# Optimization experiments

Hardware: AMD Instinct MI355X
Metric: run time of the kernel (lower is better)

Reference implementation:

```python
import jax, jax.numpy as jnp
import numpy as np

N_HEADS = 16
N_UNITS = 1024
B, S = 4, 1024


def setup_inputs() -> dict:
    key = jax.random.key(0)
    ks = jax.random.split(key, 12)
    std = 0.02
    query = jax.random.normal(ks[0], (B, S, N_UNITS), dtype=jnp.float32)
    key_t = jax.random.normal(ks[1], (B, S, N_UNITS), dtype=jnp.float32)
    value = jax.random.normal(ks[2], (B, S, N_UNITS), dtype=jnp.float32)
    # causal mask [B, S, S]; forward does mask.unsqueeze(1) -> broadcast over heads
    mask = jnp.broadcast_to(jnp.tril(jnp.ones((S, S), dtype=jnp.int32)), (B, S, S))
    Wq = jax.random.normal(ks[3], (N_UNITS, N_UNITS), dtype=jnp.float32) * std
    bq = jnp.zeros((N_UNITS,), dtype=jnp.float32)
    Wk = jax.random.normal(ks[4], (N_UNITS, N_UNITS), dtype=jnp.float32) * std
    bk = jnp.zeros((N_UNITS,), dtype=jnp.float32)
    Wv = jax.random.normal(ks[5], (N_UNITS, N_UNITS), dtype=jnp.float32) * std
    bv = jnp.zeros((N_UNITS,), dtype=jnp.float32)
    Wo = jax.random.normal(ks[6], (N_UNITS, N_UNITS), dtype=jnp.float32) * std
    bo = jnp.zeros((N_UNITS,), dtype=jnp.float32)
    return {"query": query, "key": key_t, "value": value, "mask": mask,
            "Wq": Wq, "bq": bq, "Wk": Wk, "bk": bk, "Wv": Wv, "bv": bv,
            "Wo": Wo, "bo": bo}


def reference(query, key, value, mask, Wq, bq, Wk, bk, Wv, bv, Wo, bo):
    b, s, u = query.shape
    h = N_HEADS
    dk = u // h
    # projections (torch Linear: x @ W.T + b), split into heads -> [b, h, s, dk]
    q = (query @ Wq.T + bq).reshape(b, s, h, dk).transpose(0, 2, 1, 3)
    k = (key @ Wk.T + bk).reshape(b, s, h, dk).transpose(0, 2, 1, 3)
    v = (value @ Wv.T + bv).reshape(b, s, h, dk).transpose(0, 2, 1, 3)
    # NOTE: original divides by sqrt(d_k) twice -> net scale 1/d_k (faithful)
    scores = jnp.einsum('bhqd,bhkd->bhqk', q, k) / jnp.float32(dk)
    scores = jnp.where(mask[:, None, :, :] == 0, jnp.float32(-1e9), scores)
    attn = jax.nn.softmax(scores, axis=-1)  # dropout = identity (eval mode)
    out = jnp.einsum('bhqk,bhkd->bhqd', attn, v)
    out = out.transpose(0, 2, 1, 3).reshape(b, s, u)
    return out @ Wo.T + bo
```

## Files before the change

kernel.cpp:

```cpp
#include <hip/hip_runtime.h>
#include <stdint.h>

#define NH 16
#define DK 64
#define NB 4
#define SS 1024
#define UU 1024

typedef __attribute__((ext_vector_type(8))) __bf16 bf16x8;
typedef __attribute__((ext_vector_type(4))) float f32x4;

__device__ inline short f2bf(float f) {
  union { float f; uint32_t u; } c; c.f = f;
  uint32_t u = c.u;
  uint32_t r = (u + 0x7fffu + ((u >> 16) & 1u)) >> 16;
  return (short)(uint16_t)r;
}

__global__ void cvt_multi(const float* __restrict__ s0, const float* __restrict__ s1,
                          const float* __restrict__ s2, const float* __restrict__ s3,
                          short* __restrict__ dst, int n4each) {
  const int z = blockIdx.z;
  const float* s = (z == 0) ? s0 : (z == 1) ? s1 : (z == 2) ? s2 : s3;
  int i = blockIdx.x * blockDim.x + threadIdx.x;
  if (i >= n4each) return;
  const float4 v = reinterpret_cast<const float4*>(s)[i];
  short4 o;
  o.x = f2bf(v.x); o.y = f2bf(v.y); o.z = f2bf(v.z); o.w = f2bf(v.w);
  reinterpret_cast<short4*>(dst + (size_t)z * n4each * 4)[i] = o;
}

template <int ROWS>
__device__ inline void stage_rows(short* lds, const short* gsrc, int ld) {
  const int t = threadIdx.x;
  const int w = t >> 6;
  constexpr int ROUNDS = ROWS / 64;
#pragma unroll
  for (int r = 0; r < ROUNDS; ++r) {
    int idx = r * 256 + t;
    const short* src = gsrc + (size_t)(idx >> 2) * ld + (idx & 3) * 8;
    __builtin_amdgcn_global_load_lds(
        (const __attribute__((address_space(1))) void*)src,
        (__attribute__((address_space(3))) void*)(lds + (size_t)(r * 256 + (w << 6)) * 8),
        16, 0, 0);
  }
}

#define BK 32
#define QSCALE 0.015625f

__global__ void gemm_qkv(const float* __restrict__ xq, const float* __restrict__ xk,
                         const float* __restrict__ xv, const short* __restrict__ wq,
                         const short* __restrict__ wk, const short* __restrict__ wv,
                         const float* __restrict__ bq, const float* __restrict__ bk,
                         const float* __restrict__ bv, short* __restrict__ qb,
                         short* __restrict__ kb, short* __restrict__ vT) {
  __shared__ short As[128 * BK];
  __shared__ short Bs[128 * BK];
  const int bid = blockIdx.x;
  const int g = bid & 7, s2 = bid >> 3;
  const int P = g + (s2 >> 3) * 8;
  const int xt = s2 & 7;
  const int which = P >> 5;
  const int m0 = (P & 31) * 128;
  const int n0 = xt * 128;

  const float* A = (which == 0) ? xq : (which == 1) ? xk : xv;
  const short* Bt = ((which == 0) ? wq : (which == 1) ? wk : wv) + (size_t)n0 * UU;
  const float* bias = (which == 0) ? bq : (which == 1) ? bk : bv;

  const int t = threadIdx.x;
  const int w = t >> 6, l = t & 63, lg = l >> 4, lr = l & 15;
  const int wr = w >> 1, wc = w & 1;

  f32x4 acc[4][4];
#pragma unroll
  for (int i = 0; i < 4; ++i)
#pragma unroll
    for (int j = 0; j < 4; ++j) acc[i][j] = (f32x4){0.f, 0.f, 0.f, 0.f};

  float4 ar[2][2];
  auto loadA = [&](int k0) {
#pragma unroll
    for (int r = 0; r < 2; ++r) {
      const int idx = r * 256 + t;
      const float* s = A + (size_t)(m0 + (idx >> 2)) * UU + k0 + (idx & 3) * 8;
      ar[r][0] = reinterpret_cast<const float4*>(s)[0];
      ar[r][1] = reinterpret_cast<const float4*>(s)[1];
    }
  };
  loadA(0);

  for (int k0 = 0; k0 < UU; k0 += BK) {
    asm volatile("s_waitcnt vmcnt(0)" ::: "memory");
    __builtin_amdgcn_sched_barrier(0);
#pragma unroll
    for (int r = 0; r < 2; ++r) {
      const int idx = r * 256 + t;
      bf16x8 os;
      os[0] = (__bf16)ar[r][0].x; os[1] = (__bf16)ar[r][0].y;
      os[2] = (__bf16)ar[r][0].z; os[3] = (__bf16)ar[r][0].w;
      os[4] = (__bf16)ar[r][1].x; os[5] = (__bf16)ar[r][1].y;
      os[6] = (__bf16)ar[r][1].z; os[7] = (__bf16)ar[r][1].w;
      *reinterpret_cast<bf16x8*>(&As[idx * 8]) = os;
    }
    __builtin_amdgcn_sched_barrier(0);
    stage_rows<128>(Bs, Bt + k0, UU);
    __builtin_amdgcn_sched_barrier(0);
    const int kn = k0 + BK;
    if (kn < UU) {
      loadA(kn);
      __builtin_amdgcn_sched_barrier(0);
      asm volatile("s_waitcnt vmcnt(4) lgkmcnt(0)" ::: "memory");
    } else {
      asm volatile("s_waitcnt vmcnt(0) lgkmcnt(0)" ::: "memory");
    }
    __builtin_amdgcn_sched_barrier(0);
    __builtin_amdgcn_s_barrier();
    __builtin_amdgcn_sched_barrier(0);

    bf16x8 af[4], bfr[4];
#pragma unroll
    for (int i = 0; i < 4; ++i)
      af[i] = *(const bf16x8*)&As[(wr * 64 + i * 16 + lr) * BK + lg * 8];
#pragma unroll
    for (int j = 0; j < 4; ++j)
      bfr[j] = *(const bf16x8*)&Bs[(wc * 64 + j * 16 + lr) * BK + lg * 8];
#pragma unroll
    for (int i = 0; i < 4; ++i)
#pragma unroll
      for (int j = 0; j < 4; ++j)
        acc[i][j] = __builtin_amdgcn_mfma_f32_16x16x32_bf16(af[i], bfr[j], acc[i][j], 0, 0, 0);
    __builtin_amdgcn_sched_barrier(0);
    __builtin_amdgcn_s_barrier();
  }

#pragma unroll
  for (int i = 0; i < 4; ++i) {
#pragma unroll
    for (int j = 0; j < 4; ++j) {
      const int col = n0 + wc * 64 + j * 16 + lr;
      const float bv2 = bias[col];
#pragma unroll
      for (int r = 0; r < 4; ++r) {
        const int row = m0 + wr * 64 + i * 16 + lg * 4 + r;
        float v = acc[i][j][r] + bv2;
        if (which == 0) v *= QSCALE;
        const int b = row >> 10, s = row & 1023;
        const int h = col >> 6, d = col & 63;
        if (which < 2) {
          short* outp = (which == 0) ? qb : kb;
          outp[((size_t)(b * NH + h) * SS + s) * DK + d] = f2bf(v);
        } else {
          vT[((size_t)(b * NH + h) * DK + d) * SS + s] = f2bf(v);
        }
      }
    }
  }
}

__global__ void gemm_out(const short* __restrict__ A, const short* __restrict__ Bt,
                         const float* __restrict__ bias, float* __restrict__ out,
                         int M, int N, int K) {
  __shared__ short As[128 * BK];
  __shared__ short Bs[64 * BK];
  const int bid = blockIdx.x;
  const int g = bid & 7, s2 = bid >> 3;
  const int y = g + (s2 >> 4) * 8;
  const int xt = s2 & 15;
  const int m0 = y * 128, n0 = xt * 64;

  const int t = threadIdx.x;
  const int w = t >> 6, l = t & 63, lg = l >> 4, lr = l & 15;
  const int wr = w >> 1, wc = w & 1;

  f32x4 acc[4][2];
#pragma unroll
  for (int i = 0; i < 4; ++i)
#pragma unroll
    for (int j = 0; j < 2; ++j) acc[i][j] = (f32x4){0.f, 0.f, 0.f, 0.f};

  for (int k0 = 0; k0 < K; k0 += BK) {
    stage_rows<128>(As, A + (size_t)m0 * K + k0, K);
    stage_rows<64>(Bs, Bt + (size_t)n0 * K + k0, K);
    __syncthreads();
    bf16x8 af[4], bfr[2];
#pragma unroll
    for (int i = 0; i < 4; ++i)
      af[i] = *(const bf16x8*)&As[(wr * 64 + i * 16 + lr) * BK + lg * 8];
#pragma unroll
    for (int j = 0; j < 2; ++j)
      bfr[j] = *(const bf16x8*)&Bs[(wc * 32 + j * 16 + lr) * BK + lg * 8];
#pragma unroll
    for (int i = 0; i < 4; ++i)
#pragma unroll
      for (int j = 0; j < 2; ++j)
        acc[i][j] = __builtin_amdgcn_mfma_f32_16x16x32_bf16(af[i], bfr[j], acc[i][j], 0, 0, 0);
    __syncthreads();
  }

#pragma unroll
  for (int i = 0; i < 4; ++i) {
#pragma unroll
    for (int j = 0; j < 2; ++j) {
      const int col = n0 + wc * 32 + j * 16 + lr;
      const float bv = bias[col];
#pragma unroll
      for (int r = 0; r < 4; ++r) {
        const int row = m0 + wr * 64 + i * 16 + lg * 4 + r;
        out[(size_t)row * N + col] = acc[i][j][r] + bv;
      }
    }
  }
}

__global__ void attn_fused(const short* __restrict__ Qh, const short* __restrict__ Kh,
                           const short* __restrict__ VT, short* __restrict__ Ctx) {
  __shared__ short Ks[2][4096];
  __shared__ short Vs[2][4096];
  __shared__ short Pl[4][1024];

  const int bid = blockIdx.x;
  const int g = bid & 7, s2 = bid >> 3;
  const int bh = g + (s2 >> 3) * 8;
  const int xp = s2 & 7;

  const int t = threadIdx.x;
  const int w = t >> 6, l = t & 63, lg = l >> 4, lr = l & 15;
  const short* Qp = Qh + (size_t)bh * SS * DK;
  const short* Kp = Kh + (size_t)bh * SS * DK;
  const short* Vp = VT + (size_t)bh * DK * SS;
  short* Pw = Pl[w];
  const int b = bh >> 4, h = bh & 15;
  const int rowloc = w * 16 + lg * 4;

  int lofs[2], gofK[2], gofV[2];
#pragma unroll
  for (int r = 0; r < 2; ++r) {
    const int idx = r * 256 + t;
    const int L = idx << 4;
    const int Lp = L ^ (((L >> 7) & 7) << 4);
    lofs[r] = (r * 256 + (w << 6)) * 8;
    gofK[r] = (Lp >> 7) * DK + ((Lp & 127) >> 1);
    gofV[r] = (Lp >> 7) * SS + ((Lp & 127) >> 1);
  }

  for (int half = 0; half < 2; ++half) {
    const int qt = half ? (15 - xp) : xp;
    const int q0 = qt * 64 + w * 16;
    const int nt = qt + 1;

    bf16x8 qf[2];
#pragma unroll
    for (int c = 0; c < 2; ++c)
      qf[c] = *(const bf16x8*)&Qp[(q0 + lr) * DK + c * 32 + lg * 8];

    f32x4 o[4];
    float lsum[4];
#pragma unroll
    for (int i = 0; i < 4; ++i) { o[i] = (f32x4){0.f, 0.f, 0.f, 0.f}; lsum[i] = 0.f; }

#pragma unroll
    for (int r = 0; r < 2; ++r)
      __builtin_amdgcn_global_load_lds(
          (const __attribute__((address_space(1))) void*)(Kp + gofK[r]),
          (__attribute__((address_space(3))) void*)(Ks[0] + lofs[r]), 16, 0, 0);
#pragma unroll
    for (int r = 0; r < 2; ++r)
      __builtin_amdgcn_global_load_lds(
          (const __attribute__((address_space(1))) void*)(Vp + gofV[r]),
          (__attribute__((address_space(3))) void*)(Vs[0] + lofs[r]), 16, 0, 0);

    for (int tt = 0; tt < nt; ++tt) {
      const int cb = tt & 1, nb = cb ^ 1;
      if (tt + 1 < nt) {
        const size_t koff = (size_t)(tt + 1) * 64;
#pragma unroll
        for (int r = 0; r < 2; ++r)
          __builtin_amdgcn_global_load_lds(
              (const __attribute__((address_space(1))) void*)(Kp + koff * DK + gofK[r]),
              (__attribute__((address_space(3))) void*)(Ks[nb] + lofs[r]), 16, 0, 0);
#pragma unroll
        for (int r = 0; r < 2; ++r)
          __builtin_amdgcn_global_load_lds(
              (const __attribute__((address_space(1))) void*)(Vp + koff + gofV[r]),
              (__attribute__((address_space(3))) void*)(Vs[nb] + lofs[r]), 16, 0, 0);
        asm volatile("s_waitcnt vmcnt(4)" ::: "memory");
      } else {
        asm volatile("s_waitcnt vmcnt(0)" ::: "memory");
      }
      __builtin_amdgcn_sched_barrier(0);
      __builtin_amdgcn_s_barrier();
      __builtin_amdgcn_sched_barrier(0);

      const short* Kt = Ks[cb];
      const short* Vt = Vs[cb];

      f32x4 sacc[4];
#pragma unroll
      for (int nf = 0; nf < 4; ++nf) sacc[nf] = (f32x4){0.f, 0.f, 0.f, 0.f};
#pragma unroll
      for (int nf = 0; nf < 4; ++nf)
#pragma unroll
        for (int c = 0; c < 2; ++c) {
          const int row = nf * 16 + lr;
          const int Lb = (row << 7) + c * 64 + lg * 16;
          bf16x8 kf = *(const bf16x8*)((const char*)Kt + (Lb ^ ((row & 7) << 4)));
          sacc[nf] = __builtin_amdgcn_mfma_f32_16x16x32_bf16(qf[c], kf, sacc[nf], 0, 0, 0);
        }

      const bool diag = (tt == qt);
#pragma unroll
      for (int nf = 0; nf < 4; ++nf) {
        const int colloc = nf * 16 + lr;
#pragma unroll
        for (int r = 0; r < 4; ++r) {
          float s = sacc[nf][r];
          if (diag && colloc > (rowloc + r)) s = -1.0e9f;
          float p = __expf(s);
          lsum[r] += p;
          const int prow = lg * 4 + r;
          const int boff = (prow * 128 + colloc * 2) ^ ((prow & 7) << 4);
          Pw[boff >> 1] = f2bf(p);
        }
      }

      asm volatile("s_waitcnt lgkmcnt(0)" ::: "memory");
      __builtin_amdgcn_sched_barrier(0);

      bf16x8 pf[2];
#pragma unroll
      for (int c2 = 0; c2 < 2; ++c2) {
        const int boff = (lr * 128 + (c2 * 32 + lg * 8) * 2) ^ ((lr & 7) << 4);
        pf[c2] = *(const bf16x8*)((const char*)Pw + boff);
      }
#pragma unroll
      for (int df = 0; df < 4; ++df)
#pragma unroll
        for (int c2 = 0; c2 < 2; ++c2) {
          const int row = df * 16 + lr;
          const int Lb = (row << 7) + c2 * 64 + lg * 16;
          bf16x8 vf = *(const bf16x8*)((const char*)Vt + (Lb ^ ((row & 7) << 4)));
          o[df] = __builtin_amdgcn_mfma_f32_16x16x32_bf16(pf[c2], vf, o[df], 0, 0, 0);
        }
      __builtin_amdgcn_sched_barrier(0);
      __builtin_amdgcn_s_barrier();
    }

#pragma unroll
    for (int r = 0; r < 4; ++r) {
#pragma unroll
      for (int d = 1; d < 16; d <<= 1)
        lsum[r] += __shfl_xor(lsum[r], d, 64);
    }
    float inv[4];
#pragma unroll
    for (int r = 0; r < 4; ++r) inv[r] = 1.0f / lsum[r];
#pragma unroll
    for (int df = 0; df < 4; ++df)
#pragma unroll
      for (int r = 0; r < 4; ++r) {
        const int qg = q0 + lg * 4 + r;
        Ctx[((size_t)(b * SS + qg)) * UU + h * DK + df * 16 + lr] = f2bf(o[df][r] * inv[r]);
      }
  }
}

extern "C" void kernel_launch(void* const* d_in, const int* in_sizes, int n_in,
                              void* d_out, int out_size, void* d_ws, size_t ws_size,
                              hipStream_t stream) {
  const float* query = (const float*)d_in[0];
  const float* key   = (const float*)d_in[1];
  const float* value = (const float*)d_in[2];
  const float* Wq = (const float*)d_in[4];
  const float* bq = (const float*)d_in[5];
  const float* Wk = (const float*)d_in[6];
  const float* bk = (const float*)d_in[7];
  const float* Wv = (const float*)d_in[8];
  const float* bv = (const float*)d_in[9];
  const float* Wo = (const float*)d_in[10];
  const float* bo = (const float*)d_in[11];
  float* out = (float*)d_out;

  char* ws = (char*)d_ws;
  const size_t MT = (size_t)NB * SS;
  short* qb  = (short*)ws;
  short* kb  = qb + MT * UU;
  short* vT  = kb + MT * UU;
  short* ctx = vT + MT * UU;
  short* wq  = ctx + MT * UU;
  short* wk  = wq + (size_t)UU * UU;
  short* wv  = wk + (size_t)UU * UU;
  short* wo  = wv + (size_t)UU * UU;

  const int TPB = 256;
  {
    int n4 = (int)((size_t)UU * UU / 4);
    hipLaunchKernelGGL(cvt_multi, dim3(n4 / TPB, 1, 4), dim3(TPB), 0, stream,
                       Wq, Wk, Wv, Wo, wq, n4);
  }

  hipLaunchKernelGGL(gemm_qkv, dim3(768), dim3(TPB), 0, stream,
                     query, key, value, wq, wk, wv, bq, bk, bv, qb, kb, vT);

  hipLaunchKernelGGL(attn_fused, dim3(512), dim3(TPB), 0, stream, qb, kb, vT, ctx);

  hipLaunchKernelGGL(gemm_out, dim3(512), dim3(TPB), 0, stream,
                     ctx, wo, bo, out, (int)MT, UU, UU);
}
```

Measured before the change: 218.8 us.

## Double-buffer LDS tiles in projection GEMMs to overlap loads with MFMA

Both the QKV projection GEMM and the output projection GEMM now keep two LDS buffers for the A and B tiles, plus ping-pong register buffers for the fp32 A tiles. Each iteration waits once, issues the next tile's global-to-LDS loads, then runs the MFMAs on the current buffer, which removes the second barrier per k-step. The goal is to hide global load latency behind compute. In exchange LDS use doubles, which may lower occupancy, and the tighter waitcnt ordering carries some risk of a race.

```diff
diff --git a/kernel.cpp b/kernel.cpp
--- a/kernel.cpp
+++ b/kernel.cpp
@@ -55,8 +55,8 @@
                          const float* __restrict__ bq, const float* __restrict__ bk,
                          const float* __restrict__ bv, short* __restrict__ qb,
                          short* __restrict__ kb, short* __restrict__ vT) {
-  __shared__ short As[128 * BK];
-  __shared__ short Bs[128 * BK];
+  __shared__ short As0[128 * BK], As1[128 * BK];
+  __shared__ short Bs0[128 * BK], Bs1[128 * BK];
   const int bid = blockIdx.x;
   const int g = bid & 7, s2 = bid >> 3;
   const int P = g + (s2 >> 3) * 8;
@@ -79,8 +79,9 @@
 #pragma unroll
     for (int j = 0; j < 4; ++j) acc[i][j] = (f32x4){0.f, 0.f, 0.f, 0.f};
 
-  float4 ar[2][2];
-  auto loadA = [&](int k0) {
+  float4 arE[2][2], arO[2][2];
+
+  auto loadA = [&](float4 (&ar)[2][2], int k0) {
 #pragma unroll
     for (int r = 0; r < 2; ++r) {
       const int idx = r * 256 + t;
@@ -89,50 +90,51 @@
       ar[r][1] = reinterpret_cast<const float4*>(s)[1];
     }
   };
-  loadA(0);
-
-  for (int k0 = 0; k0 < UU; k0 += BK) {
+
+  auto body = [&](float4 (&arC)[2][2], float4 (&arN)[2][2],
+                  short* AsC, short* BsC, short* BsN, int kn) {
     asm volatile("s_waitcnt vmcnt(0)" ::: "memory");
     __builtin_amdgcn_sched_barrier(0);
 #pragma unroll
     for (int r = 0; r < 2; ++r) {
       const int idx = r * 256 + t;
       bf16x8 os;
-      os[0] = (__bf16)ar[r][0].x; os[1] = (__bf16)ar[r][0].y;
-      os[2] = (__bf16)ar[r][0].z; os[3] = (__bf16)ar[r][0].w;
-      os[4] = (__bf16)ar[r][1].x; os[5] = (__bf16)ar[r][1].y;
-      os[6] = (__bf16)ar[r][1].z; os[7] = (__bf16)ar[r][1].w;
-      *reinterpret_cast<bf16x8*>(&As[idx * 8]) = os;
-    }
-    __builtin_amdgcn_sched_barrier(0);
-    stage_rows<128>(Bs, Bt + k0, UU);
-    __builtin_amdgcn_sched_barrier(0);
-    const int kn = k0 + BK;
+      os[0] = (__bf16)arC[r][0].x; os[1] = (__bf16)arC[r][0].y;
+      os[2] = (__bf16)arC[r][0].z; os[3] = (__bf16)arC[r][0].w;
+      os[4] = (__bf16)arC[r][1].x; os[5] = (__bf16)arC[r][1].y;
+      os[6] = (__bf16)arC[r][1].z; os[7] = (__bf16)arC[r][1].w;
+      *reinterpret_cast<bf16x8*>(&AsC[idx * 8]) = os;
+    }
+    __builtin_amdgcn_sched_barrier(0);
+    asm volatile("s_waitcnt lgkmcnt(0)" ::: "memory");
+    __builtin_amdgcn_sched_barrier(0);
+    __builtin_amdgcn_s_barrier();
+    __builtin_amdgcn_sched_barrier(0);
     if (kn < UU) {
-      loadA(kn);
-      __builtin_amdgcn_sched_barrier(0);
-      asm volatile("s_waitcnt vmcnt(4) lgkmcnt(0)" ::: "memory");
-    } else {
-      asm volatile("s_waitcnt vmcnt(0) lgkmcnt(0)" ::: "memory");
-    }
-    __builtin_amdgcn_sched_barrier(0);
-    __builtin_amdgcn_s_barrier();
-    __builtin_amdgcn_sched_barrier(0);
-
+      loadA(arN, kn);
+      stage_rows<128>(BsN, Bt + kn, UU);
+    }
+    __builtin_amdgcn_sched_barrier(0);
     bf16x8 af[4], bfr[4];
 #pragma unroll
     for (int i = 0; i < 4; ++i)
-      af[i] = *(const bf16x8*)&As[(wr * 64 + i * 16 + lr) * BK + lg * 8];
+      af[i] = *(const bf16x8*)&AsC[(wr * 64 + i * 16 + lr) * BK + lg * 8];
 #pragma unroll
     for (int j = 0; j < 4; ++j)
-      bfr[j] = *(const bf16x8*)&Bs[(wc * 64 + j * 16 + lr) * BK + lg * 8];
+      bfr[j] = *(const bf16x8*)&BsC[(wc * 64 + j * 16 + lr) * BK + lg * 8];
 #pragma unroll
     for (int i = 0; i < 4; ++i)
 #pragma unroll
       for (int j = 0; j < 4; ++j)
         acc[i][j] = __builtin_amdgcn_mfma_f32_16x16x32_bf16(af[i], bfr[j], acc[i][j], 0, 0, 0);
     __builtin_amdgcn_sched_barrier(0);
-    __builtin_amdgcn_s_barrier();
+  };
+
+  loadA(arE, 0);
+  stage_rows<128>(Bs0, Bt, UU);
+  for (int k0 = 0; k0 < UU; k0 += 2 * BK) {
+    body(arE, arO, As0, Bs0, Bs1, k0 + BK);
+    body(arO, arE, As1, Bs1, Bs0, k0 + 2 * BK);
   }
 
 #pragma unroll
@@ -162,8 +164,8 @@
 __global__ void gemm_out(const short* __restrict__ A, const short* __restrict__ Bt,
                          const float* __restrict__ bias, float* __restrict__ out,
                          int M, int N, int K) {
-  __shared__ short As[128 * BK];
-  __shared__ short Bs[64 * BK];
+  __shared__ short As0[128 * BK], As1[128 * BK];
+  __shared__ short Bs0[64 * BK], Bs1[64 * BK];
   const int bid = blockIdx.x;
   const int g = bid & 7, s2 = bid >> 3;
   const int y = g + (s2 >> 4) * 8;
@@ -180,23 +182,37 @@
 #pragma unroll
     for (int j = 0; j < 2; ++j) acc[i][j] = (f32x4){0.f, 0.f, 0.f, 0.f};
 
-  for (int k0 = 0; k0 < K; k0 += BK) {
-    stage_rows<128>(As, A + (size_t)m0 * K + k0, K);
-    stage_rows<64>(Bs, Bt + (size_t)n0 * K + k0, K);
-    __syncthreads();
+  auto stage = [&](short* AsD, short* BsD, int k0) {
+    stage_rows<128>(AsD, A + (size_t)m0 * K + k0, K);
+    stage_rows<64>(BsD, Bt + (size_t)n0 * K + k0, K);
+  };
+
+  auto body = [&](short* AsC, short* BsC, short* AsN, short* BsN, int kn) {
+    asm volatile("s_waitcnt vmcnt(0)" ::: "memory");
+    __builtin_amdgcn_sched_barrier(0);
+    __builtin_amdgcn_s_barrier();
+    __builtin_amdgcn_sched_barrier(0);
+    if (kn < K) stage(AsN, BsN, kn);
+    __builtin_amdgcn_sched_barrier(0);
     bf16x8 af[4], bfr[2];
 #pragma unroll
     for (int i = 0; i < 4; ++i)
-      af[i] = *(const bf16x8*)&As[(wr * 64 + i * 16 + lr) * BK + lg * 8];
+      af[i] = *(const bf16x8*)&AsC[(wr * 64 + i * 16 + lr) * BK + lg * 8];
 #pragma unroll
     for (int j = 0; j < 2; ++j)
-      bfr[j] = *(const bf16x8*)&Bs[(wc * 32 + j * 16 + lr) * BK + lg * 8];
+      bfr[j] = *(const bf16x8*)&BsC[(wc * 32 + j * 16 + lr) * BK + lg * 8];
 #pragma unroll
     for (int i = 0; i < 4; ++i)
 #pragma unroll
       for (int j = 0; j < 2; ++j)
         acc[i][j] = __builtin_amdgcn_mfma_f32_16x16x32_bf16(af[i], bfr[j], acc[i][j], 0, 0, 0);
-    __syncthreads();
+    __builtin_amdgcn_sched_barrier(0);
+  };
+
+  stage(As0, Bs0, 0);
+  for (int k0 = 0; k0 < K; k0 += 2 * BK) {
+    body(As0, Bs0, As1, Bs1, k0 + BK);
+    body(As1, Bs1, As0, Bs0, k0 + 2 * BK);
   }
 
 #pragma unroll
```

Result: slower. 271.7 us (+24.1%).

## Software-pipeline QKV and output GEMMs with triple-buffered LDS and prefetch depth two

Applied to the files above, without the earlier changes.

Both projection GEMMs now prefetch two K-tiles ahead. B tiles (and A tiles in gemm_out) go to a three-slot LDS ring, and QKV's fp32 A data ping-pongs between two register sets and two LDS buffers. Fine-grained vmcnt waits and a single barrier per iteration replace the previous syncthreads pairs. The goal is to hide global load latency behind MFMA work, at the cost of more LDS and register use, which may reduce occupancy.

```diff
diff --git a/kernel.cpp b/kernel.cpp
--- a/kernel.cpp
+++ b/kernel.cpp
@@ -49,14 +49,63 @@
 #define BK 32
 #define QSCALE 0.015625f
 
+
+#define LOADAQ(A00, A01, A10, A11, KO)                                        \
+  {                                                                           \
+    const float* sA_ = A + (size_t)(m0 + (t >> 2)) * UU + (KO) + (t & 3) * 8; \
+    A00 = reinterpret_cast<const float4*>(sA_)[0];                            \
+    A01 = reinterpret_cast<const float4*>(sA_)[1];                            \
+    const float* sB_ = A + (size_t)(m0 + 64 + (t >> 2)) * UU + (KO) + (t & 3) * 8; \
+    A10 = reinterpret_cast<const float4*>(sB_)[0];                            \
+    A11 = reinterpret_cast<const float4*>(sB_)[1];                            \
+  }
+
+#define STAGEBQ(BI) stage_rows<128>(BsAll + ((BI) % 3) * (128 * BK), Bt + (BI) * BK, UU);
+
+#define BODYQ(A00, A01, A10, A11, AS, BI, VMC, ...)                           \
+  {                                                                           \
+    asm volatile("s_waitcnt vmcnt(" VMC ")" ::: "memory");                    \
+    __builtin_amdgcn_sched_barrier(0);                                        \
+    {                                                                         \
+      bf16x8 os_;                                                             \
+      os_[0] = (__bf16)A00.x; os_[1] = (__bf16)A00.y;                         \
+      os_[2] = (__bf16)A00.z; os_[3] = (__bf16)A00.w;                         \
+      os_[4] = (__bf16)A01.x; os_[5] = (__bf16)A01.y;                         \
+      os_[6] = (__bf16)A01.z; os_[7] = (__bf16)A01.w;                         \
+      *reinterpret_cast<bf16x8*>(&(AS)[t * 8]) = os_;                         \
+      os_[0] = (__bf16)A10.x; os_[1] = (__bf16)A10.y;                         \
+      os_[2] = (__bf16)A10.z; os_[3] = (__bf16)A10.w;                         \
+      os_[4] = (__bf16)A11.x; os_[5] = (__bf16)A11.y;                         \
+      os_[6] = (__bf16)A11.z; os_[7] = (__bf16)A11.w;                         \
+      *reinterpret_cast<bf16x8*>(&(AS)[(256 + t) * 8]) = os_;                 \
+    }                                                                         \
+    __builtin_amdgcn_sched_barrier(0);                                        \
+    asm volatile("s_waitcnt lgkmcnt(0)" ::: "memory");                        \
+    __builtin_amdgcn_s_barrier();                                             \
+    __builtin_amdgcn_sched_barrier(0);                                        \
+    __VA_ARGS__                                                               \
+    __builtin_amdgcn_sched_barrier(0);                                        \
+    {                                                                         \
+      const short* BsC_ = BsAll + ((BI) % 3) * (128 * BK);                    \
+      bf16x8 af[4], bfr[4];                                                   \
+      _Pragma("unroll") for (int i = 0; i < 4; ++i)                           \
+          af[i] = *(const bf16x8*)&(AS)[(wr * 64 + i * 16 + lr) * BK + lg * 8]; \
+      _Pragma("unroll") for (int j = 0; j < 4; ++j)                           \
+          bfr[j] = *(const bf16x8*)&BsC_[(wc * 64 + j * 16 + lr) * BK + lg * 8]; \
+      _Pragma("unroll") for (int i = 0; i < 4; ++i)                           \
+          _Pragma("unroll") for (int j = 0; j < 4; ++j)                       \
+              acc[i][j] = __builtin_amdgcn_mfma_f32_16x16x32_bf16(af[i], bfr[j], acc[i][j], 0, 0, 0); \
+    }                                                                         \
+  }
+
 __global__ void gemm_qkv(const float* __restrict__ xq, const float* __restrict__ xk,
                          const float* __restrict__ xv, const short* __restrict__ wq,
                          const short* __restrict__ wk, const short* __restrict__ wv,
                          const float* __restrict__ bq, const float* __restrict__ bk,
                          const float* __restrict__ bv, short* __restrict__ qb,
                          short* __restrict__ kb, short* __restrict__ vT) {
-  __shared__ short As[128 * BK];
-  __shared__ short Bs[128 * BK];
+  __shared__ short As0[128 * BK], As1[128 * BK];
+  __shared__ short BsAll[3 * 128 * BK];
   const int bid = blockIdx.x;
   const int g = bid & 7, s2 = bid >> 3;
   const int P = g + (s2 >> 3) * 8;
@@ -79,61 +128,20 @@
 #pragma unroll
     for (int j = 0; j < 4; ++j) acc[i][j] = (f32x4){0.f, 0.f, 0.f, 0.f};
 
-  float4 ar[2][2];
-  auto loadA = [&](int k0) {
-#pragma unroll
-    for (int r = 0; r < 2; ++r) {
-      const int idx = r * 256 + t;
-      const float* s = A + (size_t)(m0 + (idx >> 2)) * UU + k0 + (idx & 3) * 8;
-      ar[r][0] = reinterpret_cast<const float4*>(s)[0];
-      ar[r][1] = reinterpret_cast<const float4*>(s)[1];
-    }
-  };
-  loadA(0);
-
-  for (int k0 = 0; k0 < UU; k0 += BK) {
-    asm volatile("s_waitcnt vmcnt(0)" ::: "memory");
-    __builtin_amdgcn_sched_barrier(0);
-#pragma unroll
-    for (int r = 0; r < 2; ++r) {
-      const int idx = r * 256 + t;
-      bf16x8 os;
-      os[0] = (__bf16)ar[r][0].x; os[1] = (__bf16)ar[r][0].y;
-      os[2] = (__bf16)ar[r][0].z; os[3] = (__bf16)ar[r][0].w;
-      os[4] = (__bf16)ar[r][1].x; os[5] = (__bf16)ar[r][1].y;
-      os[6] = (__bf16)ar[r][1].z; os[7] = (__bf16)ar[r][1].w;
-      *reinterpret_cast<bf16x8*>(&As[idx * 8]) = os;
-    }
-    __builtin_amdgcn_sched_barrier(0);
-    stage_rows<128>(Bs, Bt + k0, UU);
-    __builtin_amdgcn_sched_barrier(0);
-    const int kn = k0 + BK;
-    if (kn < UU) {
-      loadA(kn);
-      __builtin_amdgcn_sched_barrier(0);
-      asm volatile("s_waitcnt vmcnt(4) lgkmcnt(0)" ::: "memory");
-    } else {
-      asm volatile("s_waitcnt vmcnt(0) lgkmcnt(0)" ::: "memory");
-    }
-    __builtin_amdgcn_sched_barrier(0);
-    __builtin_amdgcn_s_barrier();
-    __builtin_amdgcn_sched_barrier(0);
-
-    bf16x8 af[4], bfr[4];
-#pragma unroll
-    for (int i = 0; i < 4; ++i)
-      af[i] = *(const bf16x8*)&As[(wr * 64 + i * 16 + lr) * BK + lg * 8];
-#pragma unroll
-    for (int j = 0; j < 4; ++j)
-      bfr[j] = *(const bf16x8*)&Bs[(wc * 64 + j * 16 + lr) * BK + lg * 8];
-#pragma unroll
-    for (int i = 0; i < 4; ++i)
-#pragma unroll
-      for (int j = 0; j < 4; ++j)
-        acc[i][j] = __builtin_amdgcn_mfma_f32_16x16x32_bf16(af[i], bfr[j], acc[i][j], 0, 0, 0);
-    __builtin_amdgcn_sched_barrier(0);
-    __builtin_amdgcn_s_barrier();
-  }
+  float4 aE0, aE1, aE2, aE3;
+  float4 aO0, aO1, aO2, aO3;
+
+  LOADAQ(aE0, aE1, aE2, aE3, 0); STAGEBQ(0);
+  LOADAQ(aO0, aO1, aO2, aO3, BK); STAGEBQ(1);
+
+  for (int bi = 0; bi < 30; bi += 2) {
+    BODYQ(aE0, aE1, aE2, aE3, As0, bi, "6",
+          LOADAQ(aE0, aE1, aE2, aE3, (bi + 2) * BK); STAGEBQ(bi + 2);)
+    BODYQ(aO0, aO1, aO2, aO3, As1, bi + 1, "6",
+          LOADAQ(aO0, aO1, aO2, aO3, (bi + 3) * BK); STAGEBQ(bi + 3);)
+  }
+  BODYQ(aE0, aE1, aE2, aE3, As0, 30, "6", ;)
+  BODYQ(aO0, aO1, aO2, aO3, As1, 31, "0", ;)
 
 #pragma unroll
   for (int i = 0; i < 4; ++i) {
@@ -159,11 +167,39 @@
   }
 }
 
+#define STAGEO(BI)                                                            \
+  {                                                                           \
+    stage_rows<128>(AsAll + ((BI) % 3) * (128 * BK), A + (size_t)m0 * K + (BI) * BK, K); \
+    stage_rows<64>(BsAll3 + ((BI) % 3) * (64 * BK), Bt + (size_t)n0 * K + (BI) * BK, K); \
+  }
+
+#define BODYO(BI, VMC, ...)                                                   \
+  {                                                                           \
+    asm volatile("s_waitcnt vmcnt(" VMC ")" ::: "memory");                    \
+    __builtin_amdgcn_sched_barrier(0);                                        \
+    __builtin_amdgcn_s_barrier();                                             \
+    __builtin_amdgcn_sched_barrier(0);                                        \
+    __VA_ARGS__                                                               \
+    __builtin_amdgcn_sched_barrier(0);                                        \
+    {                                                                         \
+      const short* AsC_ = AsAll + ((BI) % 3) * (128 * BK);                    \
+      const short* BsC_ = BsAll3 + ((BI) % 3) * (64 * BK);                    \
+      bf16x8 af[4], bfr[2];                                                   \
+      _Pragma("unroll") for (int i = 0; i < 4; ++i)                           \
+          af[i] = *(const bf16x8*)&AsC_[(wr * 64 + i * 16 + lr) * BK + lg * 8]; \
+      _Pragma("unroll") for (int j = 0; j < 2; ++j)                           \
+          bfr[j] = *(const bf16x8*)&BsC_[(wc * 32 + j * 16 + lr) * BK + lg * 8]; \
+      _Pragma("unroll") for (int i = 0; i < 4; ++i)                           \
+          _Pragma("unroll") for (int j = 0; j < 2; ++j)                       \
+              acc[i][j] = __builtin_amdgcn_mfma_f32_16x16x32_bf16(af[i], bfr[j], acc[i][j], 0, 0, 0); \
+    }                                                                         \
+  }
+
 __global__ void gemm_out(const short* __restrict__ A, const short* __restrict__ Bt,
                          const float* __restrict__ bias, float* __restrict__ out,
                          int M, int N, int K) {
-  __shared__ short As[128 * BK];
-  __shared__ short Bs[64 * BK];
+  __shared__ short AsAll[3 * 128 * BK];
+  __shared__ short BsAll3[3 * 64 * BK];
   const int bid = blockIdx.x;
   const int g = bid & 7, s2 = bid >> 3;
   const int y = g + (s2 >> 4) * 8;
@@ -180,24 +216,13 @@
 #pragma unroll
     for (int j = 0; j < 2; ++j) acc[i][j] = (f32x4){0.f, 0.f, 0.f, 0.f};
 
-  for (int k0 = 0; k0 < K; k0 += BK) {
-    stage_rows<128>(As, A + (size_t)m0 * K + k0, K);
-    stage_rows<64>(Bs, Bt + (size_t)n0 * K + k0, K);
-    __syncthreads();
-    bf16x8 af[4], bfr[2];
-#pragma unroll
-    for (int i = 0; i < 4; ++i)
-      af[i] = *(const bf16x8*)&As[(wr * 64 + i * 16 + lr) * BK + lg * 8];
-#pragma unroll
-    for (int j = 0; j < 2; ++j)
-      bfr[j] = *(const bf16x8*)&Bs[(wc * 32 + j * 16 + lr) * BK + lg * 8];
-#pragma unroll
-    for (int i = 0; i < 4; ++i)
-#pragma unroll
-      for (int j = 0; j < 2; ++j)
-        acc[i][j] = __builtin_amdgcn_mfma_f32_16x16x32_bf16(af[i], bfr[j], acc[i][j], 0, 0, 0);
-    __syncthreads();
-  }
+  STAGEO(0);
+  STAGEO(1);
+  for (int bi = 0; bi < 30; ++bi) {
+    BODYO(bi, "3", STAGEO(bi + 2);)
+  }
+  BODYO(30, "3", ;)
+  BODYO(31, "0", ;)
 
 #pragma unroll
   for (int i = 0; i < 4; ++i) {
```

Result: slower. 482.0 us (+120.2%).

## Pre-convert activations to bf16, double-buffer LDS with BK=64 and XOR swizzle

Applied to the files above, without the earlier changes.

Activation inputs are now converted to bf16 in one combined conversion kernel together with the weights, so gemm_qkv stages both operands through async global_load_lds instead of loading and converting fp32 in registers. Both projection GEMMs move to BK=64 with double-buffered LDS tiles, prefetching the next K-slice while computing the current one and halving barrier count. An XOR swizzle on the LDS layout is meant to avoid bank conflicts on fragment reads. In exchange there is an extra full round trip of the bf16 activations through memory and a larger workspace, and LDS per block doubles, which may lower occupancy.

```diff
diff --git a/kernel.cpp b/kernel.cpp
--- a/kernel.cpp
+++ b/kernel.cpp
@@ -17,28 +17,40 @@
   return (short)(uint16_t)r;
 }
 
-__global__ void cvt_multi(const float* __restrict__ s0, const float* __restrict__ s1,
-                          const float* __restrict__ s2, const float* __restrict__ s3,
-                          short* __restrict__ dst, int n4each) {
-  const int z = blockIdx.z;
-  const float* s = (z == 0) ? s0 : (z == 1) ? s1 : (z == 2) ? s2 : s3;
-  int i = blockIdx.x * blockDim.x + threadIdx.x;
-  if (i >= n4each) return;
-  const float4 v = reinterpret_cast<const float4*>(s)[i];
+__global__ void cvt_all(const float* __restrict__ q, const float* __restrict__ k,
+                        const float* __restrict__ v, const float* __restrict__ wq,
+                        const float* __restrict__ wk, const float* __restrict__ wv,
+                        const float* __restrict__ wo, short* __restrict__ dst) {
+  const int i = blockIdx.x * blockDim.x + threadIdx.x;
+  const float* s;
+  int local;
+  if (i < 3 * 1048576) {
+    const int z = i >> 20;
+    local = i & 1048575;
+    s = (z == 0) ? q : (z == 1) ? k : v;
+  } else {
+    const int j = i - 3 * 1048576;
+    const int z = j >> 18;
+    local = j & 262143;
+    s = (z == 0) ? wq : (z == 1) ? wk : (z == 2) ? wv : wo;
+  }
+  const float4 vv = reinterpret_cast<const float4*>(s)[local];
   short4 o;
-  o.x = f2bf(v.x); o.y = f2bf(v.y); o.z = f2bf(v.z); o.w = f2bf(v.w);
-  reinterpret_cast<short4*>(dst + (size_t)z * n4each * 4)[i] = o;
+  o.x = f2bf(vv.x); o.y = f2bf(vv.y); o.z = f2bf(vv.z); o.w = f2bf(vv.w);
+  reinterpret_cast<short4*>(dst)[i] = o;
 }
 
 template <int ROWS>
-__device__ inline void stage_rows(short* lds, const short* gsrc, int ld) {
+__device__ inline void stage_swz(short* lds, const short* gsrc, int ld) {
   const int t = threadIdx.x;
   const int w = t >> 6;
-  constexpr int ROUNDS = ROWS / 64;
+  constexpr int ROUNDS = ROWS * 8 / 256;
 #pragma unroll
   for (int r = 0; r < ROUNDS; ++r) {
-    int idx = r * 256 + t;
-    const short* src = gsrc + (size_t)(idx >> 2) * ld + (idx & 3) * 8;
+    const int idx = r * 256 + t;
+    const int L = idx << 4;
+    const int Lp = L ^ (((L >> 7) & 7) << 4);
+    const short* src = gsrc + (size_t)(Lp >> 7) * ld + ((Lp & 127) >> 1);
     __builtin_amdgcn_global_load_lds(
         (const __attribute__((address_space(1))) void*)src,
         (__attribute__((address_space(3))) void*)(lds + (size_t)(r * 256 + (w << 6)) * 8),
@@ -46,17 +58,22 @@
   }
 }
 
-#define BK 32
+#define BK 64
 #define QSCALE 0.015625f
 
-__global__ void gemm_qkv(const float* __restrict__ xq, const float* __restrict__ xk,
-                         const float* __restrict__ xv, const short* __restrict__ wq,
+__device__ inline bf16x8 frag_swz(const short* base, int row, int kbyte) {
+  const int byte = (row << 7) + kbyte;
+  return *(const bf16x8*)((const char*)base + (byte ^ ((row & 7) << 4)));
+}
+
+__global__ void gemm_qkv(const short* __restrict__ xq, const short* __restrict__ xk,
+                         const short* __restrict__ xv, const short* __restrict__ wq,
                          const short* __restrict__ wk, const short* __restrict__ wv,
                          const float* __restrict__ bq, const float* __restrict__ bk,
                          const float* __restrict__ bv, short* __restrict__ qb,
                          short* __restrict__ kb, short* __restrict__ vT) {
-  __shared__ short As[128 * BK];
-  __shared__ short Bs[128 * BK];
+  __shared__ short AsAll[2 * 128 * BK];
+  __shared__ short BsAll[2 * 128 * BK];
   const int bid = blockIdx.x;
   const int g = bid & 7, s2 = bid >> 3;
   const int P = g + (s2 >> 3) * 8;
@@ -65,7 +82,7 @@
   const int m0 = (P & 31) * 128;
   const int n0 = xt * 128;
 
-  const float* A = (which == 0) ? xq : (which == 1) ? xk : xv;
+  const short* Abf = (which == 0) ? xq : (which == 1) ? xk : xv;
   const short* Bt = ((which == 0) ? wq : (which == 1) ? wk : wv) + (size_t)n0 * UU;
   const float* bias = (which == 0) ? bq : (which == 1) ? bk : bv;
 
@@ -79,60 +96,43 @@
 #pragma unroll
     for (int j = 0; j < 4; ++j) acc[i][j] = (f32x4){0.f, 0.f, 0.f, 0.f};
 
-  float4 ar[2][2];
-  auto loadA = [&](int k0) {
-#pragma unroll
-    for (int r = 0; r < 2; ++r) {
-      const int idx = r * 256 + t;
-      const float* s = A + (size_t)(m0 + (idx >> 2)) * UU + k0 + (idx & 3) * 8;
-      ar[r][0] = reinterpret_cast<const float4*>(s)[0];
-      ar[r][1] = reinterpret_cast<const float4*>(s)[1];
-    }
-  };
-  loadA(0);
-
-  for (int k0 = 0; k0 < UU; k0 += BK) {
-    asm volatile("s_waitcnt vmcnt(0)" ::: "memory");
+  stage_swz<128>(AsAll, Abf + (size_t)m0 * UU, UU);
+  stage_swz<128>(BsAll, Bt, UU);
+  asm volatile("s_waitcnt vmcnt(0)" ::: "memory");
+  __builtin_amdgcn_s_barrier();
+  __builtin_amdgcn_sched_barrier(0);
+
+  for (int bi = 0; bi < 16; ++bi) {
+    const int cur = bi & 1;
+    const short* AsC = AsAll + cur * (128 * BK);
+    const short* BsC = BsAll + cur * (128 * BK);
+    if (bi + 1 < 16) {
+      const int nxt = cur ^ 1;
+      stage_swz<128>(AsAll + nxt * (128 * BK), Abf + (size_t)m0 * UU + (bi + 1) * BK, UU);
+      stage_swz<128>(BsAll + nxt * (128 * BK), Bt + (bi + 1) * BK, UU);
+    }
     __builtin_amdgcn_sched_barrier(0);
 #pragma unroll
-    for (int r = 0; r < 2; ++r) {
-      const int idx = r * 256 + t;
-      bf16x8 os;
-      os[0] = (__bf16)ar[r][0].x; os[1] = (__bf16)ar[r][0].y;
-      os[2] = (__bf16)ar[r][0].z; os[3] = (__bf16)ar[r][0].w;
-      os[4] = (__bf16)ar[r][1].x; os[5] = (__bf16)ar[r][1].y;
-      os[6] = (__bf16)ar[r][1].z; os[7] = (__bf16)ar[r][1].w;
-      *reinterpret_cast<bf16x8*>(&As[idx * 8]) = os;
-    }
-    __builtin_amdgcn_sched_barrier(0);
-    stage_rows<128>(Bs, Bt + k0, UU);
-    __builtin_amdgcn_sched_barrier(0);
-    const int kn = k0 + BK;
-    if (kn < UU) {
-      loadA(kn);
-      __builtin_amdgcn_sched_barrier(0);
-      asm volatile("s_waitcnt vmcnt(4) lgkmcnt(0)" ::: "memory");
-    } else {
-      asm volatile("s_waitcnt vmcnt(0) lgkmcnt(0)" ::: "memory");
-    }
-    __builtin_amdgcn_sched_barrier(0);
-    __builtin_amdgcn_s_barrier();
-    __builtin_amdgcn_sched_barrier(0);
-
-    bf16x8 af[4], bfr[4];
-#pragma unroll
-    for (int i = 0; i < 4; ++i)
-      af[i] = *(const bf16x8*)&As[(wr * 64 + i * 16 + lr) * BK + lg * 8];
-#pragma unroll
-    for (int j = 0; j < 4; ++j)
-      bfr[j] = *(const bf16x8*)&Bs[(wc * 64 + j * 16 + lr) * BK + lg * 8];
-#pragma unroll
-    for (int i = 0; i < 4; ++i)
+    for (int kk = 0; kk < 2; ++kk) {
+      bf16x8 af[4], bfr[4];
+#pragma unroll
+      for (int i = 0; i < 4; ++i)
+        af[i] = frag_swz(AsC, wr * 64 + i * 16 + lr, kk * 64 + lg * 16);
 #pragma unroll
       for (int j = 0; j < 4; ++j)
-        acc[i][j] = __builtin_amdgcn_mfma_f32_16x16x32_bf16(af[i], bfr[j], acc[i][j], 0, 0, 0);
-    __builtin_amdgcn_sched_barrier(0);
-    __builtin_amdgcn_s_barrier();
+        bfr[j] = frag_swz(BsC, wc * 64 + j * 16 + lr, kk * 64 + lg * 16);
+#pragma unroll
+      for (int i = 0; i < 4; ++i)
+#pragma unroll
+        for (int j = 0; j < 4; ++j)
+          acc[i][j] = __builtin_amdgcn_mfma_f32_16x16x32_bf16(af[i], bfr[j], acc[i][j], 0, 0, 0);
+    }
+    if (bi + 1 < 16) {
+      __builtin_amdgcn_sched_barrier(0);
+      asm volatile("s_waitcnt vmcnt(0)" ::: "memory");
+      __builtin_amdgcn_s_barrier();
+      __builtin_amdgcn_sched_barrier(0);
+    }
   }
 
 #pragma unroll
@@ -162,8 +162,8 @@
 __global__ void gemm_out(const short* __restrict__ A, const short* __restrict__ Bt,
                          const float* __restrict__ bias, float* __restrict__ out,
                          int M, int N, int K) {
-  __shared__ short As[128 * BK];
-  __shared__ short Bs[64 * BK];
+  __shared__ short AsAll[2 * 128 * BK];
+  __shared__ short BsAll3[2 * 64 * BK];
   const int bid = blockIdx.x;
   const int g = bid & 7, s2 = bid >> 3;
   const int y = g + (s2 >> 4) * 8;
@@ -180,23 +180,43 @@
 #pragma unroll
     for (int j = 0; j < 2; ++j) acc[i][j] = (f32x4){0.f, 0.f, 0.f, 0.f};
 
-  for (int k0 = 0; k0 < K; k0 += BK) {
-    stage_rows<128>(As, A + (size_t)m0 * K + k0, K);
-    stage_rows<64>(Bs, Bt + (size_t)n0 * K + k0, K);
-    __syncthreads();
-    bf16x8 af[4], bfr[2];
-#pragma unroll
-    for (int i = 0; i < 4; ++i)
-      af[i] = *(const bf16x8*)&As[(wr * 64 + i * 16 + lr) * BK + lg * 8];
-#pragma unroll
-    for (int j = 0; j < 2; ++j)
-      bfr[j] = *(const bf16x8*)&Bs[(wc * 32 + j * 16 + lr) * BK + lg * 8];
-#pragma unroll
-    for (int i = 0; i < 4; ++i)
+  stage_swz<128>(AsAll, A + (size_t)m0 * K, K);
+  stage_swz<64>(BsAll3, Bt + (size_t)n0 * K, K);
+  asm volatile("s_waitcnt vmcnt(0)" ::: "memory");
+  __builtin_amdgcn_s_barrier();
+  __builtin_amdgcn_sched_barrier(0);
+
+  for (int bi = 0; bi < 16; ++bi) {
+    const int cur = bi & 1;
+    const short* AsC = AsAll + cur * (128 * BK);
+    const short* BsC = BsAll3 + cur * (64 * BK);
+    if (bi + 1 < 16) {
+      const int nxt = cur ^ 1;
+      stage_swz<128>(AsAll + nxt * (128 * BK), A + (size_t)m0 * K + (bi + 1) * BK, K);
+      stage_swz<64>(BsAll3 + nxt * (64 * BK), Bt + (size_t)n0 * K + (bi + 1) * BK, K);
+    }
+    __builtin_amdgcn_sched_barrier(0);
+#pragma unroll
+    for (int kk = 0; kk < 2; ++kk) {
+      bf16x8 af[4], bfr[2];
+#pragma unroll
+      for (int i = 0; i < 4; ++i)
+        af[i] = frag_swz(AsC, wr * 64 + i * 16 + lr, kk * 64 + lg * 16);
 #pragma unroll
       for (int j = 0; j < 2; ++j)
-        acc[i][j] = __builtin_amdgcn_mfma_f32_16x16x32_bf16(af[i], bfr[j], acc[i][j], 0, 0, 0);
-    __syncthreads();
+        bfr[j] = frag_swz(BsC, wc * 32 + j * 16 + lr, kk * 64 + lg * 16);
+#pragma unroll
+      for (int i = 0; i < 4; ++i)
+#pragma unroll
+        for (int j = 0; j < 2; ++j)
+          acc[i][j] = __builtin_amdgcn_mfma_f32_16x16x32_bf16(af[i], bfr[j], acc[i][j], 0, 0, 0);
+    }
+    if (bi + 1 < 16) {
+      __builtin_amdgcn_sched_barrier(0);
+      asm volatile("s_waitcnt vmcnt(0)" ::: "memory");
+      __builtin_amdgcn_s_barrier();
+      __builtin_amdgcn_sched_barrier(0);
+    }
   }
 
 #pragma unroll
@@ -388,20 +408,20 @@
   short* kb  = qb + MT * UU;
   short* vT  = kb + MT * UU;
   short* ctx = vT + MT * UU;
-  short* wq  = ctx + MT * UU;
+  short* xq  = ctx + MT * UU;
+  short* xk  = xq + MT * UU;
+  short* xv  = xk + MT * UU;
+  short* wq  = xv + MT * UU;
   short* wk  = wq + (size_t)UU * UU;
   short* wv  = wk + (size_t)UU * UU;
   short* wo  = wv + (size_t)UU * UU;
 
   const int TPB = 256;
-  {
-    int n4 = (int)((size_t)UU * UU / 4);
-    hipLaunchKernelGGL(cvt_multi, dim3(n4 / TPB, 1, 4), dim3(TPB), 0, stream,
-                       Wq, Wk, Wv, Wo, wq, n4);
-  }
+  hipLaunchKernelGGL(cvt_all, dim3(4194304 / TPB), dim3(TPB), 0, stream,
+                     query, key, value, Wq, Wk, Wv, Wo, xq);
 
   hipLaunchKernelGGL(gemm_qkv, dim3(768), dim3(TPB), 0, stream,
-                     query, key, value, wq, wk, wv, bq, bk, bv, qb, kb, vT);
+                     xq, xk, xv, wq, wk, wv, bq, bk, bv, qb, kb, vT);
 
   hipLaunchKernelGGL(attn_fused, dim3(512), dim3(TPB), 0, stream, qb, kb, vT, ctx);
 
```

Result: no change. 218.7 us (-0.1%).
